# Optimization experiments

Hardware: AMD Instinct MI355X
Metric: run time of the kernel (lower is better)

Reference implementation:

```python
import jax, jax.numpy as jnp
import numpy as np

N_DRUG, N_PROT = 20000, 8000
D_DRUG, D_PROT = 300, 1280
HIDDEN, OUT = 512, 5
N_EDGE, N_LBL = 500000, 200000


def setup_inputs() -> dict:
    key = jax.random.key(0)
    ks = jax.random.split(key, 12)
    inp = {
        "x_drug": jax.random.normal(ks[0], (N_DRUG, D_DRUG), dtype=jnp.float32),
        "x_prot": jax.random.normal(ks[1], (N_PROT, D_PROT), dtype=jnp.float32),
        "edge_src": jax.random.randint(ks[2], (N_EDGE,), 0, N_DRUG, dtype=jnp.int32),
        "edge_dst": jax.random.randint(ks[3], (N_EDGE,), 0, N_PROT, dtype=jnp.int32),
        "lbl_src": jax.random.randint(ks[4], (N_LBL,), 0, N_DRUG, dtype=jnp.int32),
        "lbl_dst": jax.random.randint(ks[5], (N_LBL,), 0, N_PROT, dtype=jnp.int32),
        # SAGEConv params: lin_l (on aggregated src msgs, with bias), lin_r (on dst, no bias)
        "W_l": jax.random.normal(ks[6], (HIDDEN, D_DRUG), dtype=jnp.float32) / np.sqrt(D_DRUG),
        "b_l": jnp.zeros((HIDDEN,), dtype=jnp.float32),
        "W_r": jax.random.normal(ks[7], (HIDDEN, D_PROT), dtype=jnp.float32) / np.sqrt(D_PROT),
        # final edge classifier Linear(D_DRUG + HIDDEN, OUT)
        "W_lin": jax.random.normal(ks[8], (OUT, D_DRUG + HIDDEN), dtype=jnp.float32) / np.sqrt(D_DRUG + HIDDEN),
        "b_lin": jnp.zeros((OUT,), dtype=jnp.float32),
    }
    return inp


def reference(x_drug, x_prot, edge_src, edge_dst, lbl_src, lbl_dst,
              W_l, b_l, W_r, W_lin, b_lin):
    # --- bipartite SAGEConv((drug, protein)) with default mean aggregation ---
    msg = x_drug[edge_src]                                   # [E, D_DRUG] gather
    agg = jax.ops.segment_sum(msg, edge_dst, num_segments=N_PROT)   # [N_PROT, D_DRUG]
    cnt = jax.ops.segment_sum(jnp.ones((edge_dst.shape[0],), jnp.float32),
                              edge_dst, num_segments=N_PROT)
    mean = agg / jnp.clip(cnt, 1.0, None)[:, None]           # mean over in-neighbors
    prot_emb_all = mean @ W_l.T + b_l + x_prot @ W_r.T       # [N_PROT, HIDDEN]

    # --- gather endpoints for labeled edges, concat, linear ---
    drug_emb = x_drug[lbl_src]                               # [L, D_DRUG]
    prot_emb = prot_emb_all[lbl_dst]                         # [L, HIDDEN]
    edge_emb = jnp.concatenate([drug_emb, prot_emb], axis=1) # [L, D_DRUG+HIDDEN]
    return edge_emb @ W_lin.T + b_lin                        # [L, OUT]
```

## Files before the change

### kernel.cpp

```cpp
#include <hip/hip_runtime.h>

#define N_DRUG 20000
#define N_PROT 8000
#define D_DRUG 300
#define D_PROT 1280
#define HIDDEN 512
#define OUT_D  5
#define N_EDGE 500000
#define N_LBL  200000
#define WLD    812
#define AGG_S  8
#define PA_S   8

#define PGROUPS 16
#define PROT_PER_G (N_PROT / PGROUPS)
#define ESLICES 64
#define EDGE_PER_S 8192
#define SCAN_B (PGROUPS * ESLICES)
#define PART_STRIDE (N_PROT * 6)

__global__ void k_fold(const float* __restrict__ W_l, const float* __restrict__ W_r,
                       const float* __restrict__ W_lin, const float* __restrict__ b_l,
                       float* __restrict__ A, float* __restrict__ B, float* __restrict__ c) {
    int t  = blockIdx.x * 256 + threadIdx.x;
    int e  = t >> 3;
    int j  = t & 7;
    int h0 = j * 64;
    const int nA = OUT_D * D_DRUG;
    const int nB = OUT_D * D_PROT;
    float s = 0.f;
    if (e < nA) {
        int o = e / D_DRUG, k = e - o * D_DRUG;
        const float* wp = W_lin + o * WLD + D_DRUG + h0;
        const float* w  = W_l + (size_t)h0 * D_DRUG + k;
#pragma unroll 8
        for (int h = 0; h < 64; ++h) s += wp[h] * w[h * D_DRUG];
    } else if (e < nA + nB) {
        int u = e - nA;
        int o = u / D_PROT, k = u - o * D_PROT;
        const float* wp = W_lin + o * WLD + D_DRUG + h0;
        const float* w  = W_r + (size_t)h0 * D_PROT + k;
#pragma unroll 8
        for (int h = 0; h < 64; ++h) s += wp[h] * w[h * D_PROT];
    } else if (e < nA + nB + OUT_D) {
        int o = e - nA - nB;
        const float* wp = W_lin + o * WLD + D_DRUG + h0;
#pragma unroll 8
        for (int h = 0; h < 64; ++h) s += wp[h] * b_l[h0 + h];
    }
    s += __shfl_xor(s, 1, 64);
    s += __shfl_xor(s, 2, 64);
    s += __shfl_xor(s, 4, 64);
    if (j == 0) {
        if (e < nA)                     A[e] = s;
        else if (e < nA + nB)           B[e - nA] = s;
        else if (e < nA + nB + OUT_D)   c[e - nA - nB] = s;
    }
}

__global__ void k_drug(const float* __restrict__ x_drug, const float* __restrict__ A,
                       const float* __restrict__ W_lin, const float* __restrict__ b_lin,
                       float* __restrict__ P_A, float* __restrict__ drugO) {
    int gid = blockIdx.x * 256 + threadIdx.x;
    int row = gid >> 4;
    int sub = threadIdx.x & 15;
    const float4* xr = (const float4*)(x_drug + (size_t)row * D_DRUG);
    float acc[10];
#pragma unroll
    for (int i = 0; i < 10; ++i) acc[i] = 0.f;
    for (int k = sub; k < D_DRUG / 4; k += 16) {
        float4 x = xr[k];
#pragma unroll
        for (int o = 0; o < OUT_D; ++o) {
            float4 a = ((const float4*)(A + o * D_DRUG))[k];
            acc[o] += x.x * a.x + x.y * a.y + x.z * a.z + x.w * a.w;
            float4 w = ((const float4*)(W_lin + o * WLD))[k];
            acc[5 + o] += x.x * w.x + x.y * w.y + x.z * w.z + x.w * w.w;
        }
    }
#pragma unroll
    for (int i = 0; i < 10; ++i) {
        float v = acc[i];
        for (int m = 8; m; m >>= 1) v += __shfl_xor(v, m, 64);
        acc[i] = v;
    }
    if (sub < OUT_D) {
        P_A[(size_t)row * PA_S + sub]    = acc[sub];
        drugO[(size_t)row * OUT_D + sub] = acc[5 + sub] + b_lin[sub];
    } else if (sub < PA_S) {
        P_A[(size_t)row * PA_S + sub] = 0.f;
    }
}

__global__ void k_scan_prot(const float* __restrict__ x_prot,
                            const int* __restrict__ edge_src, const int* __restrict__ edge_dst,
                            const float* __restrict__ B, const float* __restrict__ c,
                            const float* __restrict__ P_A, float* __restrict__ partial,
                            float* __restrict__ protO) {
    int b = blockIdx.x;
    if (b < SCAN_B) {
        __shared__ float lagg[PROT_PER_G * 6];
        int tid = threadIdx.x;
        for (int i = tid; i < PROT_PER_G * 6; i += 256) lagg[i] = 0.f;
        __syncthreads();

        int pg  = b >> 6;
        int sl  = b & 63;
        int plo = pg * PROT_PER_G;
        int e0  = sl * EDGE_PER_S;
        const int4* dst4 = (const int4*)edge_dst;
        const int4* src4 = (const int4*)edge_src;

#define ACCUM(dd, ss) do {                                                   \
            int _d = (dd) - plo;                                             \
            if ((unsigned)_d < (unsigned)PROT_PER_G) {                       \
                const float* pp = P_A + (size_t)(ss) * PA_S;                 \
                float4 p4 = *(const float4*)pp;                              \
                float  p5 = pp[4];                                           \
                float* L = lagg + _d * 6;                                    \
                atomicAdd(L + 0, p4.x);                                      \
                atomicAdd(L + 1, p4.y);                                      \
                atomicAdd(L + 2, p4.z);                                      \
                atomicAdd(L + 3, p4.w);                                      \
                atomicAdd(L + 4, p5);                                        \
                atomicAdd(L + 5, 1.0f);                                      \
            } } while (0)

#pragma unroll
        for (int it = 0; it < EDGE_PER_S / 1024; ++it) {
            int e = e0 + (it * 256 + tid) * 4;
            if (e < N_EDGE) {
                int4 d4 = dst4[e >> 2];
                int4 s4 = src4[e >> 2];
                ACCUM(d4.x, s4.x);
                ACCUM(d4.y, s4.y);
                ACCUM(d4.z, s4.z);
                ACCUM(d4.w, s4.w);
            }
        }
#undef ACCUM
        __syncthreads();
        float* pout = partial + (size_t)sl * PART_STRIDE + (size_t)plo * 6;
        for (int i = tid; i < PROT_PER_G * 6; i += 256) pout[i] = lagg[i];
    } else {
        int wave = ((b - SCAN_B) * 256 + threadIdx.x) >> 6;
        int lane = threadIdx.x & 63;
        const float4* xr = (const float4*)(x_prot + (size_t)wave * D_PROT);
        float acc[OUT_D] = {0.f, 0.f, 0.f, 0.f, 0.f};
        for (int k = lane; k < D_PROT / 4; k += 64) {
            float4 x = xr[k];
#pragma unroll
            for (int o = 0; o < OUT_D; ++o) {
                float4 bb = ((const float4*)(B + o * D_PROT))[k];
                acc[o] += x.x * bb.x + x.y * bb.y + x.z * bb.z + x.w * bb.w;
            }
        }
#pragma unroll
        for (int o = 0; o < OUT_D; ++o) {
            float v = acc[o];
            for (int off = 32; off; off >>= 1) v += __shfl_xor(v, off, 64);
            acc[o] = v;
        }
        if (lane < OUT_D) protO[(size_t)wave * OUT_D + lane] = acc[lane] + c[lane];
    }
}

__global__ void k_reduce(const float* __restrict__ partial, float* __restrict__ agg) {
    int tid = threadIdx.x;
    int gid = blockIdx.x * 240 + tid;
    float s = 0.f;
#pragma unroll 8
    for (int sl = 0; sl < ESLICES; ++sl) s += partial[(size_t)sl * PART_STRIDE + gid];
    __shared__ float tmp[240];
    tmp[tid] = s;
    __syncthreads();
    int j = tid % 6;
    if (j < 5) {
        float cnt = tmp[tid - j + 5];
        agg[(size_t)(gid / 6) * AGG_S + j] = s / fmaxf(cnt, 1.0f);
    }
}

__global__ void k_final(const int* __restrict__ lbl_src, const int* __restrict__ lbl_dst,
                        const float* __restrict__ drugO, const float* __restrict__ protO,
                        const float* __restrict__ agg, float* __restrict__ out) {
    int l = blockIdx.x * blockDim.x + threadIdx.x;
    if (l >= N_LBL) return;
    int s = lbl_src[l], d = lbl_dst[l];
    const float* dr = &drugO[(size_t)s * OUT_D];
    const float* pr = &protO[(size_t)d * OUT_D];
    const float* ag = &agg[(size_t)d * AGG_S];
    float4 m4 = *(const float4*)ag;
    float  m5 = ag[4];
    float* op = &out[(size_t)l * OUT_D];
    op[0] = dr[0] + pr[0] + m4.x;
    op[1] = dr[1] + pr[1] + m4.y;
    op[2] = dr[2] + pr[2] + m4.z;
    op[3] = dr[3] + pr[3] + m4.w;
    op[4] = dr[4] + pr[4] + m5;
}

extern "C" void kernel_launch(void* const* d_in, const int* in_sizes, int n_in,
                              void* d_out, int out_size, void* d_ws, size_t ws_size,
                              hipStream_t stream) {
    const float* x_drug   = (const float*)d_in[0];
    const float* x_prot   = (const float*)d_in[1];
    const int*   edge_src = (const int*)d_in[2];
    const int*   edge_dst = (const int*)d_in[3];
    const int*   lbl_src  = (const int*)d_in[4];
    const int*   lbl_dst  = (const int*)d_in[5];
    const float* W_l      = (const float*)d_in[6];
    const float* b_l      = (const float*)d_in[7];
    const float* W_r      = (const float*)d_in[8];
    const float* W_lin    = (const float*)d_in[9];
    const float* b_lin    = (const float*)d_in[10];
    float* out = (float*)d_out;

    char* ws = (char*)d_ws;
    float* agg     = (float*)(ws + 0);
    float* A       = (float*)(ws + 256000);
    float* B       = (float*)(ws + 262000);
    float* c       = (float*)(ws + 287600);
    float* P_A     = (float*)(ws + 287632);
    float* drugO   = (float*)(ws + 927632);
    float* protO   = (float*)(ws + 1327632);
    float* partial = (float*)(ws + 1487632);

    k_fold<<<248, 256, 0, stream>>>(W_l, W_r, W_lin, b_l, A, B, c);
    k_drug<<<1250, 256, 0, stream>>>(x_drug, A, W_lin, b_lin, P_A, drugO);
    k_scan_prot<<<SCAN_B + 2000, 256, 0, stream>>>(x_prot, edge_src, edge_dst,
                                                   B, c, P_A, partial, protO);
    k_reduce<<<200, 240, 0, stream>>>(partial, agg);
    k_final<<<(N_LBL + 255) / 256, 256, 0, stream>>>(lbl_src, lbl_dst, drugO, protO, agg, out);
}
```

Measured before the change: 164.4 us.

## Fuse five kernel launches into one cooperative persistent kernel with grid syncs

Replaces the chain of five kernel launches (fold, drug projection, edge scan plus protein projection, reduce, final gather) with a single cooperative kernel of 1024 blocks. Each stage runs as a grid-stride loop over the old block indices, and grid.sync separates the stages. This removes the per-launch overhead and the gaps between kernels. It also halves the number of edge slices (32 instead of 64), which cuts partial-buffer traffic in the reduce stage but gives each scan block more edges. If the cooperative launch fails, the code falls back to the original launches.

```diff
diff --git a/kernel.cpp b/kernel.cpp
--- a/kernel.cpp
+++ b/kernel.cpp
@@ -1,4 +1,7 @@
 #include <hip/hip_runtime.h>
+#include <hip/hip_cooperative_groups.h>
+
+namespace cg = cooperative_groups;
 
 #define N_DRUG 20000
 #define N_PROT 8000
@@ -12,12 +15,213 @@
 #define AGG_S  8
 #define PA_S   8
 
+#define MEGA_GRID 1024
+#define MPG 16
+#define MPROT_G (N_PROT / MPG)
+#define MSL 32
+#define N_EDGE4 (N_EDGE / 4)
+#define ME4_PER_S 3907
+#define MSCAN_VB (MPG * MSL)
+#define MPART_STRIDE (N_PROT * 6)
+
 #define PGROUPS 16
 #define PROT_PER_G (N_PROT / PGROUPS)
 #define ESLICES 64
 #define EDGE_PER_S 8192
 #define SCAN_B (PGROUPS * ESLICES)
 #define PART_STRIDE (N_PROT * 6)
+
+__global__ __launch_bounds__(256, 4)
+void k_mega(const float* __restrict__ x_drug, const float* __restrict__ x_prot,
+            const int* __restrict__ edge_src, const int* __restrict__ edge_dst,
+            const int* __restrict__ lbl_src, const int* __restrict__ lbl_dst,
+            const float* __restrict__ W_l, const float* __restrict__ b_l,
+            const float* __restrict__ W_r, const float* __restrict__ W_lin,
+            const float* __restrict__ b_lin,
+            float* __restrict__ A, float* __restrict__ B, float* __restrict__ c,
+            float* __restrict__ P_A, float* __restrict__ drugO,
+            float* __restrict__ protO, float* __restrict__ partial,
+            float* __restrict__ agg, float* __restrict__ out) {
+    cg::grid_group grid = cg::this_grid();
+    int tid = threadIdx.x;
+    __shared__ float smem[MPROT_G * 6];
+
+    for (int vb = blockIdx.x; vb < 248; vb += gridDim.x) {
+        int t  = vb * 256 + tid;
+        int e  = t >> 3;
+        int j  = t & 7;
+        int h0 = j * 64;
+        const int nA = OUT_D * D_DRUG;
+        const int nB = OUT_D * D_PROT;
+        float s = 0.f;
+        if (e < nA) {
+            int o = e / D_DRUG, k = e - o * D_DRUG;
+            const float* wp = W_lin + o * WLD + D_DRUG + h0;
+            const float* w  = W_l + (size_t)h0 * D_DRUG + k;
+#pragma unroll 8
+            for (int h = 0; h < 64; ++h) s += wp[h] * w[h * D_DRUG];
+        } else if (e < nA + nB) {
+            int u = e - nA;
+            int o = u / D_PROT, k = u - o * D_PROT;
+            const float* wp = W_lin + o * WLD + D_DRUG + h0;
+            const float* w  = W_r + (size_t)h0 * D_PROT + k;
+#pragma unroll 8
+            for (int h = 0; h < 64; ++h) s += wp[h] * w[h * D_PROT];
+        } else if (e < nA + nB + OUT_D) {
+            int o = e - nA - nB;
+            const float* wp = W_lin + o * WLD + D_DRUG + h0;
+#pragma unroll 8
+            for (int h = 0; h < 64; ++h) s += wp[h] * b_l[h0 + h];
+        }
+        s += __shfl_xor(s, 1, 64);
+        s += __shfl_xor(s, 2, 64);
+        s += __shfl_xor(s, 4, 64);
+        if (j == 0) {
+            if (e < nA)                     A[e] = s;
+            else if (e < nA + nB)           B[e - nA] = s;
+            else if (e < nA + nB + OUT_D)   c[e - nA - nB] = s;
+        }
+    }
+    grid.sync();
+
+    for (int vb = blockIdx.x; vb < 1250; vb += gridDim.x) {
+        int gid = vb * 256 + tid;
+        int row = gid >> 4;
+        int sub = tid & 15;
+        const float4* xr = (const float4*)(x_drug + (size_t)row * D_DRUG);
+        float acc[10];
+#pragma unroll
+        for (int i = 0; i < 10; ++i) acc[i] = 0.f;
+        for (int k = sub; k < D_DRUG / 4; k += 16) {
+            float4 x = xr[k];
+#pragma unroll
+            for (int o = 0; o < OUT_D; ++o) {
+                float4 a = ((const float4*)(A + o * D_DRUG))[k];
+                acc[o] += x.x * a.x + x.y * a.y + x.z * a.z + x.w * a.w;
+                float4 w = ((const float4*)(W_lin + o * WLD))[k];
+                acc[5 + o] += x.x * w.x + x.y * w.y + x.z * w.z + x.w * w.w;
+            }
+        }
+#pragma unroll
+        for (int i = 0; i < 10; ++i) {
+            float v = acc[i];
+            for (int m = 8; m; m >>= 1) v += __shfl_xor(v, m, 64);
+            acc[i] = v;
+        }
+        if (sub < OUT_D) {
+            P_A[(size_t)row * PA_S + sub]    = acc[sub];
+            drugO[(size_t)row * OUT_D + sub] = acc[5 + sub] + b_lin[sub];
+        } else if (sub < PA_S) {
+            P_A[(size_t)row * PA_S + sub] = 0.f;
+        }
+    }
+    grid.sync();
+
+    for (int vb = blockIdx.x; vb < MSCAN_VB + 2000; vb += gridDim.x) {
+        if (vb < MSCAN_VB) {
+            for (int i = tid; i < MPROT_G * 6; i += 256) smem[i] = 0.f;
+            __syncthreads();
+            int pg  = vb >> 5;
+            int sl  = vb & 31;
+            int plo = pg * MPROT_G;
+            int e0_4 = sl * ME4_PER_S;
+            int lim  = ME4_PER_S;
+            if (e0_4 + lim > N_EDGE4) lim = N_EDGE4 - e0_4;
+            const int4* dst4 = (const int4*)edge_dst;
+            const int4* src4 = (const int4*)edge_src;
+#define MACCUM(dd, ss) do {                                                  \
+                int _d = (dd) - plo;                                         \
+                if ((unsigned)_d < (unsigned)MPROT_G) {                      \
+                    const float* pp = P_A + (size_t)(ss) * PA_S;             \
+                    float4 p4 = *(const float4*)pp;                          \
+                    float  p5 = pp[4];                                       \
+                    float* L = smem + _d * 6;                                \
+                    atomicAdd(L + 0, p4.x);                                  \
+                    atomicAdd(L + 1, p4.y);                                  \
+                    atomicAdd(L + 2, p4.z);                                  \
+                    atomicAdd(L + 3, p4.w);                                  \
+                    atomicAdd(L + 4, p5);                                    \
+                    atomicAdd(L + 5, 1.0f);                                  \
+                } } while (0)
+#pragma unroll
+            for (int it = 0; it < 16; ++it) {
+                int off = it * 256 + tid;
+                if (off < lim) {
+                    int4 d4 = dst4[e0_4 + off];
+                    int4 s4 = src4[e0_4 + off];
+                    MACCUM(d4.x, s4.x);
+                    MACCUM(d4.y, s4.y);
+                    MACCUM(d4.z, s4.z);
+                    MACCUM(d4.w, s4.w);
+                }
+            }
+#undef MACCUM
+            __syncthreads();
+            float* pout = partial + (size_t)sl * MPART_STRIDE + (size_t)plo * 6;
+            for (int i = tid; i < MPROT_G * 6; i += 256) pout[i] = smem[i];
+            __syncthreads();
+        } else {
+            int wave = ((vb - MSCAN_VB) * 256 + tid) >> 6;
+            int lane = tid & 63;
+            const float4* xr = (const float4*)(x_prot + (size_t)wave * D_PROT);
+            float acc[OUT_D] = {0.f, 0.f, 0.f, 0.f, 0.f};
+            for (int k = lane; k < D_PROT / 4; k += 64) {
+                float4 x = xr[k];
+#pragma unroll
+                for (int o = 0; o < OUT_D; ++o) {
+                    float4 bb = ((const float4*)(B + o * D_PROT))[k];
+                    acc[o] += x.x * bb.x + x.y * bb.y + x.z * bb.z + x.w * bb.w;
+                }
+            }
+#pragma unroll
+            for (int o = 0; o < OUT_D; ++o) {
+                float v = acc[o];
+                for (int off = 32; off; off >>= 1) v += __shfl_xor(v, off, 64);
+                acc[o] = v;
+            }
+            if (lane < OUT_D) protO[(size_t)wave * OUT_D + lane] = acc[lane] + c[lane];
+        }
+    }
+    grid.sync();
+
+    for (int vb = blockIdx.x; vb < 200; vb += gridDim.x) {
+        int gid = vb * 240 + tid;
+        float s = 0.f;
+        if (tid < 240) {
+#pragma unroll 8
+            for (int sl = 0; sl < MSL; ++sl) s += partial[(size_t)sl * MPART_STRIDE + gid];
+        }
+        smem[tid] = s;
+        __syncthreads();
+        if (tid < 240) {
+            int j = tid % 6;
+            if (j < 5) {
+                float cnt = smem[tid - j + 5];
+                agg[(size_t)(gid / 6) * AGG_S + j] = s / fmaxf(cnt, 1.0f);
+            }
+        }
+        __syncthreads();
+    }
+    grid.sync();
+
+    for (int vb = blockIdx.x; vb < 782; vb += gridDim.x) {
+        int l = vb * 256 + tid;
+        if (l < N_LBL) {
+            int s = lbl_src[l], d = lbl_dst[l];
+            const float* dr = &drugO[(size_t)s * OUT_D];
+            const float* pr = &protO[(size_t)d * OUT_D];
+            const float* ag = &agg[(size_t)d * AGG_S];
+            float4 m4 = *(const float4*)ag;
+            float  m5 = ag[4];
+            float* op = &out[(size_t)l * OUT_D];
+            op[0] = dr[0] + pr[0] + m4.x;
+            op[1] = dr[1] + pr[1] + m4.y;
+            op[2] = dr[2] + pr[2] + m4.z;
+            op[3] = dr[3] + pr[3] + m4.w;
+            op[4] = dr[4] + pr[4] + m5;
+        }
+    }
+}
 
 __global__ void k_fold(const float* __restrict__ W_l, const float* __restrict__ W_r,
                        const float* __restrict__ W_lin, const float* __restrict__ b_l,
@@ -103,14 +307,12 @@
         int tid = threadIdx.x;
         for (int i = tid; i < PROT_PER_G * 6; i += 256) lagg[i] = 0.f;
         __syncthreads();
-
         int pg  = b >> 6;
         int sl  = b & 63;
         int plo = pg * PROT_PER_G;
         int e0  = sl * EDGE_PER_S;
         const int4* dst4 = (const int4*)edge_dst;
         const int4* src4 = (const int4*)edge_src;
-
 #define ACCUM(dd, ss) do {                                                   \
             int _d = (dd) - plo;                                             \
             if ((unsigned)_d < (unsigned)PROT_PER_G) {                       \
@@ -125,7 +327,6 @@
                 atomicAdd(L + 4, p5);                                        \
                 atomicAdd(L + 5, 1.0f);                                      \
             } } while (0)
-
 #pragma unroll
         for (int it = 0; it < EDGE_PER_S / 1024; ++it) {
             int e = e0 + (it * 256 + tid) * 4;
@@ -226,10 +427,23 @@
     float* protO   = (float*)(ws + 1327632);
     float* partial = (float*)(ws + 1487632);
 
-    k_fold<<<248, 256, 0, stream>>>(W_l, W_r, W_lin, b_l, A, B, c);
-    k_drug<<<1250, 256, 0, stream>>>(x_drug, A, W_lin, b_lin, P_A, drugO);
-    k_scan_prot<<<SCAN_B + 2000, 256, 0, stream>>>(x_prot, edge_src, edge_dst,
-                                                   B, c, P_A, partial, protO);
-    k_reduce<<<200, 240, 0, stream>>>(partial, agg);
-    k_final<<<(N_LBL + 255) / 256, 256, 0, stream>>>(lbl_src, lbl_dst, drugO, protO, agg, out);
-}
+    void* args[] = {
+        (void*)&x_drug, (void*)&x_prot, (void*)&edge_src, (void*)&edge_dst,
+        (void*)&lbl_src, (void*)&lbl_dst, (void*)&W_l, (void*)&b_l,
+        (void*)&W_r, (void*)&W_lin, (void*)&b_lin,
+        (void*)&A, (void*)&B, (void*)&c, (void*)&P_A, (void*)&drugO,
+        (void*)&protO, (void*)&partial, (void*)&agg, (void*)&out
+    };
+    hipError_t err = hipLaunchCooperativeKernel((void*)k_mega, dim3(MEGA_GRID),
+                                                dim3(256), args, 0, stream);
+    if (err != hipSuccess) {
+        (void)hipGetLastError();
+        k_fold<<<248, 256, 0, stream>>>(W_l, W_r, W_lin, b_l, A, B, c);
+        k_drug<<<1250, 256, 0, stream>>>(x_drug, A, W_lin, b_lin, P_A, drugO);
+        k_scan_prot<<<SCAN_B + 2000, 256, 0, stream>>>(x_prot, edge_src, edge_dst,
+                                                       B, c, P_A, partial, protO);
+        k_reduce<<<200, 240, 0, stream>>>(partial, agg);
+        k_final<<<(N_LBL + 255) / 256, 256, 0, stream>>>(lbl_src, lbl_dst, drugO,
+                                                         protO, agg, out);
+    }
+}
```

After: 585.0 us. +255.9%, slower.
